# Optimization experiments

Hardware: AMD Instinct MI355X
Metric: run time of the kernel (lower is better)

The kernel has to match this reference:

```python
import jax, jax.numpy as jnp
import numpy as np

N_NODES, N_EDGES, D = 50000, 1250000, 64
N_LAYERS = 3


def setup_inputs() -> dict:
    key = jax.random.key(0)
    ks = jax.random.split(key, 6)
    sc = 1.0 / np.sqrt(D)  # ~xavier scale for 64->64 linears
    return {
        "in_feat": jax.random.normal(ks[0], (N_NODES, D), jnp.float32),
        "src": jax.random.randint(ks[1], (N_EDGES,), 0, N_NODES, dtype=jnp.int32),
        "dst": jax.random.randint(ks[2], (N_EDGES,), 0, N_NODES, dtype=jnp.int32),
        "W_pool": jax.random.normal(ks[3], (N_LAYERS, D, D), jnp.float32) * sc,
        "b_pool": jnp.zeros((N_LAYERS, D), jnp.float32),
        "W_self": jax.random.normal(ks[4], (N_LAYERS, D, D), jnp.float32) * sc,
        "W_neigh": jax.random.normal(ks[5], (N_LAYERS, D, D), jnp.float32) * sc,
        "bias": jnp.zeros((N_LAYERS, D), jnp.float32),
    }


def reference(in_feat, src, dst, W_pool, b_pool, W_self, W_neigh, bias):
    # Dropout is identity in eval mode and omitted for determinism.
    n = in_feat.shape[0]
    h = in_feat
    for l in range(N_LAYERS):
        # per-edge pool MLP: relu(W_pool h_src + b_pool)  -> [E, D]
        m = jax.nn.relu(h[src] @ W_pool[l] + b_pool[l])
        # max-pool aggregation over incoming edges of each dst node
        agg = jax.ops.segment_max(m, dst, num_segments=n)
        # nodes with no in-edges get -inf from segment_max -> DGL uses 0
        agg = jnp.where(jnp.isfinite(agg), agg, 0.0)
        h = h @ W_self[l] + agg @ W_neigh[l] + bias[l]
        if l < N_LAYERS - 1:
            h = jax.nn.relu(h)
    return h
```

## Files before the change

kernel.cpp:

```cpp
#include <hip/hip_runtime.h>


#define NN 50000
#define NE 1250000
#define DD 64

#define BSH 7
#define NB1 391
#define CHUNK 2048
#define NBLK1 611

#define GEMM_BLOCKS 782
#define CAST_BLOCKS 400
#define NMAT 9

using bf16x8 = __attribute__((ext_vector_type(8))) short;
using f32x4  = __attribute__((ext_vector_type(4))) float;

__device__ __forceinline__ f32x4 mfma16(bf16x8 a, bf16x8 b, f32x4 c) {
    return __builtin_amdgcn_mfma_f32_16x16x32_bf16(a, b, c, 0, 0, 0);
}

__device__ __forceinline__ unsigned int f32_to_bf16_bits(float f) {
    unsigned int u = __float_as_uint(f);
    return (u + 0x7FFFu + ((u >> 16) & 1u)) >> 16;
}
__device__ __forceinline__ unsigned int pack2bf16(float a, float b) {
    return f32_to_bf16_bits(a) | (f32_to_bf16_bits(b) << 16);
}
__device__ __forceinline__ unsigned int pkmax(unsigned int a, unsigned int b) {
    unsigned int r;
    asm("v_pk_max_u16 %0, %1, %2" : "=v"(r) : "v"(a), "v"(b));
    return r;
}

__device__ __forceinline__ void load_A(const unsigned short* __restrict__ h,
                                       int row0, int lane, bf16x8& a0, bf16x8& a1) {
    int r = row0 + (lane & 15);
    int kk = (lane >> 4) * 8;
    a0 = bf16x8{0, 0, 0, 0, 0, 0, 0, 0};
    a1 = a0;
    if (r < NN) {
        a0 = *(const bf16x8*)(h + (size_t)r * DD + kk);
        a1 = *(const bf16x8*)(h + (size_t)r * DD + kk + 32);
    }
}


__global__ __launch_bounds__(256) void fat1(const int* __restrict__ dst,
                                            int* __restrict__ H,
                                            const float* __restrict__ in_feat,
                                            unsigned short* __restrict__ h0,
                                            const float* __restrict__ Wp,
                                            const float* __restrict__ Ws,
                                            const float* __restrict__ Wn,
                                            unsigned short* __restrict__ wb) {
    __shared__ int hist[NB1];
    int tid = threadIdx.x;
    int bx = blockIdx.x;
    if (bx < NBLK1) {
        for (int i = tid; i < NB1; i += 256) hist[i] = 0;
        __syncthreads();
        int base = bx * CHUNK;
        int end = min(base + CHUNK, NE);
        for (int i = base + tid; i < end; i += 256) atomicAdd(&hist[dst[i] >> BSH], 1);
        __syncthreads();
        for (int k = tid; k < NB1; k += 256) H[k * NBLK1 + bx] = hist[k];
        return;
    }
    if (bx < NBLK1 + CAST_BLOCKS) {
        const float4* inv = (const float4*)in_feat;
        uint4* ov = (uint4*)h0;
        int t = (bx - NBLK1) * 256 + tid;
        for (int u = t; u < (NN * DD) / 8; u += CAST_BLOCKS * 256) {
            float4 f0 = inv[u * 2], f1 = inv[u * 2 + 1];
            uint4 o;
            o.x = pack2bf16(f0.x, f0.y);
            o.y = pack2bf16(f0.z, f0.w);
            o.z = pack2bf16(f1.x, f1.y);
            o.w = pack2bf16(f1.z, f1.w);
            ov[u] = o;
        }
        return;
    }
    int m = bx - NBLK1 - CAST_BLOCKS;
    const float* srcW = (m < 3) ? (Wp + (size_t)m * DD * DD)
                    : (m < 6) ? (Ws + (size_t)(m - 3) * DD * DD)
                              : (Wn + (size_t)(m - 6) * DD * DD);
    unsigned short* dstW = wb + (size_t)m * 512 * 8;
    for (int idx = tid; idx < 512; idx += 256) {
        int lane = idx & 63, cc = (idx >> 6) & 3, s = idx >> 8;
        int col = cc * 16 + (lane & 15);
        int kb = s * 32 + ((lane >> 4) << 3);
#pragma unroll
        for (int j = 0; j < 8; ++j)
            dstW[idx * 8 + j] = (unsigned short)f32_to_bf16_bits(srcW[(kb + j) * DD + col]);
    }
}


__global__ __launch_bounds__(256) void fat2(const int* __restrict__ H,
                                            int* __restrict__ rowsum,
                                            int* __restrict__ colbase,
                                            int* __restrict__ ticket,
                                            const unsigned short* __restrict__ h0,
                                            const unsigned short* __restrict__ wb,
                                            const float* __restrict__ bp,
                                            unsigned short* __restrict__ z) {
    __shared__ int s[256];
    __shared__ int isLast;
    int tid = threadIdx.x;
    int bx = blockIdx.x;
    if (bx < NB1) {
        int k = bx;
        int v = 0;
        for (int b = tid; b < NBLK1; b += 256) v += H[k * NBLK1 + b];
        s[tid] = v;
        __syncthreads();
        for (int o = 128; o > 0; o >>= 1) {
            if (tid < o) s[tid] += s[tid + o];
            __syncthreads();
        }
        if (tid == 0) {
            atomicExch(&rowsum[k], s[0]);
            __threadfence();
            isLast = (atomicAdd(ticket, 1) == NB1 - 1);
        }
        __syncthreads();
        if (!isLast) return;
        if (tid < 64) {
            int running = 0;
            for (int b0 = 0; b0 < NB1; b0 += 64) {
                int idx = b0 + tid;
                int val = (idx < NB1) ? atomicAdd(&rowsum[idx], 0) : 0;
                int incl = val;
#pragma unroll
                for (int o = 1; o < 64; o <<= 1) {
                    int up = __shfl_up(incl, o);
                    if (tid >= o) incl += up;
                }
                if (idx < NB1) colbase[idx] = running + (incl - val);
                running += __shfl(incl, 63);
            }
            if (tid == 0) colbase[NB1] = running;
        }
        return;
    }
    int lane = tid & 63;
    int row0 = (bx - NB1) * 64 + (tid >> 6) * 16;
    bf16x8 a0, a1;
    load_A(h0, row0, lane, a0, a1);
    const bf16x8* WB = (const bf16x8*)wb;
    f32x4 acc[4];
#pragma unroll
    for (int c = 0; c < 4; ++c) {
        float bv = bp[c * 16 + (lane & 15)];
        acc[c] = f32x4{bv, bv, bv, bv};
        acc[c] = mfma16(a0, WB[(0 * 4 + c) * 64 + lane], acc[c]);
        acc[c] = mfma16(a1, WB[(1 * 4 + c) * 64 + lane], acc[c]);
    }
    int rbase = row0 + (lane >> 4) * 4;
#pragma unroll
    for (int reg = 0; reg < 4; ++reg) {
        int row = rbase + reg;
        if (row < NN) {
#pragma unroll
            for (int c = 0; c < 4; ++c)
                z[(size_t)row * DD + c * 16 + (lane & 15)] =
                    (unsigned short)f32_to_bf16_bits(fmaxf(acc[c][reg], 0.f));
        }
    }
}


__global__ __launch_bounds__(256) void k3_offsets(int* __restrict__ H,
                                                  const int* __restrict__ colbase) {
    int wid = (blockIdx.x * blockDim.x + threadIdx.x) >> 6;
    int lane = threadIdx.x & 63;
    if (wid >= NB1) return;
    int running = colbase[wid];
    int* row = H + wid * NBLK1;
    for (int b0 = 0; b0 < NBLK1; b0 += 64) {
        int idx = b0 + lane;
        int v = (idx < NBLK1) ? row[idx] : 0;
        int incl = v;
#pragma unroll
        for (int o = 1; o < 64; o <<= 1) {
            int up = __shfl_up(incl, o);
            if (lane >= o) incl += up;
        }
        if (idx < NBLK1) row[idx] = running + (incl - v);
        running += __shfl(incl, 63);
    }
}

__global__ __launch_bounds__(512) void p1_scatter(const int* __restrict__ dst,
                                                  const int* __restrict__ src,
                                                  const int* __restrict__ H,
                                                  int* __restrict__ pairs, int e) {
    __shared__ int off[NB1];
    __shared__ int hcnt[NB1];
    __shared__ int cursor[NB1];
    __shared__ int lbase[NB1 + 1];
    __shared__ int sorted[CHUNK];
    __shared__ int sbuf[2][512];
    int tid = threadIdx.x, bx = blockIdx.x;
    for (int i = tid; i < NB1; i += 512) {
        off[i] = H[i * NBLK1 + bx];
        hcnt[i] = 0;
        cursor[i] = 0;
    }
    __syncthreads();
    int base = bx * CHUNK;
    int end = min(base + CHUNK, e);
    int L = end - base;
    for (int i = base + tid; i < end; i += 512) atomicAdd(&hcnt[dst[i] >> BSH], 1);
    __syncthreads();
    int myv = (tid < NB1) ? hcnt[tid] : 0;
    sbuf[0][tid] = myv;
    __syncthreads();
    int cur = 0;
    for (int o = 1; o < 512; o <<= 1) {
        sbuf[cur ^ 1][tid] = sbuf[cur][tid] + ((tid >= o) ? sbuf[cur][tid - o] : 0);
        cur ^= 1;
        __syncthreads();
    }
    if (tid < NB1) lbase[tid] = sbuf[cur][tid] - myv;
    if (tid == 0) lbase[NB1] = L;
    __syncthreads();
    for (int i = base + tid; i < end; i += 512) {
        int d = dst[i];
        int k = d >> BSH;
        int r = atomicAdd(&cursor[k], 1);
        sorted[lbase[k] + r] = ((d & 127) << 16) | src[i];
    }
    __syncthreads();
    for (int t = tid; t < L; t += 512) {
        int lo = 0, hi = NB1;
        while (hi - lo > 1) {
            int mid = (lo + hi) >> 1;
            if (t >= lbase[mid]) lo = mid; else hi = mid;
        }
        pairs[off[lo] + (t - lbase[lo])] = sorted[t];
    }
}

__global__ __launch_bounds__(512) void p2_bucket(const int* __restrict__ pairs,
                                                 const int* __restrict__ colbase,
                                                 int* __restrict__ rowptr,
                                                 unsigned short* __restrict__ edge_src) {
    __shared__ int cnt[128];
    __shared__ int base2[128];
    __shared__ int cur2[128];
    __shared__ int sbuf[2][128];
    __shared__ unsigned short stage[8192];
    int k = blockIdx.x;
    int tid = threadIdx.x;
    int beg = colbase[k], end = colbase[k + 1];
    int len = end - beg;
    if (tid < 128) { cnt[tid] = 0; cur2[tid] = 0; }
    __syncthreads();
    for (int i = beg + tid; i < end; i += 512) atomicAdd(&cnt[pairs[i] >> 16], 1);
    __syncthreads();
    if (tid < 128) sbuf[0][tid] = cnt[tid];
    __syncthreads();
    int cur = 0;
    for (int o = 1; o < 128; o <<= 1) {
        if (tid < 128) sbuf[cur ^ 1][tid] = sbuf[cur][tid] + ((tid >= o) ? sbuf[cur][tid - o] : 0);
        cur ^= 1;
        __syncthreads();
    }
    if (tid < 128) {
        int excl = sbuf[cur][tid] - cnt[tid];
        base2[tid] = excl;
        int node = (k << BSH) + tid;
        if (node < NN) rowptr[node] = beg + excl;
    }
    __syncthreads();
    if (len <= 8192) {
        for (int i = beg + tid; i < end; i += 512) {
            int p = pairs[i];
            int r = atomicAdd(&cur2[p >> 16], 1);
            stage[base2[p >> 16] + r] = (unsigned short)(p & 0xFFFF);
        }
        __syncthreads();
        for (int t = tid; t < len; t += 512) edge_src[beg + t] = stage[t];
    } else {
        for (int i = beg + tid; i < end; i += 512) {
            int p = pairs[i];
            int r = atomicAdd(&cur2[p >> 16], 1);
            edge_src[beg + base2[p >> 16] + r] = (unsigned short)(p & 0xFFFF);
        }
    }
    if (k == 0 && tid == 0) rowptr[NN] = NE;
}


__global__ __launch_bounds__(256) void gemm_fused_mfma(const unsigned short* __restrict__ h,
                                                       const unsigned short* __restrict__ agg,
                                                       const unsigned short* __restrict__ wbs,
                                                       const unsigned short* __restrict__ wbn,
                                                       const unsigned short* __restrict__ wbp,
                                                       const float* __restrict__ b,
                                                       const float* __restrict__ bp,
                                                       unsigned short* __restrict__ hn_out,
                                                       unsigned short* __restrict__ z) {
    __shared__ unsigned short hnl[4][16 * 72];
    int tid = threadIdx.x;
    int w = tid >> 6, lane = tid & 63;
    int row0 = blockIdx.x * 64 + w * 16;
    bf16x8 ah0, ah1, ag0, ag1;
    load_A(h, row0, lane, ah0, ah1);
    load_A(agg, row0, lane, ag0, ag1);
    const bf16x8* WS = (const bf16x8*)wbs;
    const bf16x8* WN = (const bf16x8*)wbn;
    const bf16x8* WP = (const bf16x8*)wbp;
    f32x4 acc[4];
#pragma unroll
    for (int c = 0; c < 4; ++c) {
        float bv = b[c * 16 + (lane & 15)];
        acc[c] = f32x4{bv, bv, bv, bv};
        acc[c] = mfma16(ah0, WS[(0 * 4 + c) * 64 + lane], acc[c]);
        acc[c] = mfma16(ah1, WS[(1 * 4 + c) * 64 + lane], acc[c]);
        acc[c] = mfma16(ag0, WN[(0 * 4 + c) * 64 + lane], acc[c]);
        acc[c] = mfma16(ag1, WN[(1 * 4 + c) * 64 + lane], acc[c]);
    }
    int rloc = (lane >> 4) * 4;
    int rbase = row0 + rloc;
#pragma unroll
    for (int reg = 0; reg < 4; ++reg) {
        int row = rbase + reg;
#pragma unroll
        for (int c = 0; c < 4; ++c) {
            unsigned short us =
                (unsigned short)f32_to_bf16_bits(fmaxf(acc[c][reg], 0.f));
            hnl[w][(rloc + reg) * 72 + c * 16 + (lane & 15)] = us;
            if (row < NN) hn_out[(size_t)row * DD + c * 16 + (lane & 15)] = us;
        }
    }
    int kk = (lane >> 4) * 8;
    bf16x8 p0 = *(const bf16x8*)&hnl[w][(lane & 15) * 72 + kk];
    bf16x8 p1 = *(const bf16x8*)&hnl[w][(lane & 15) * 72 + kk + 32];
    f32x4 acc2[4];
#pragma unroll
    for (int c = 0; c < 4; ++c) {
        float bv = bp[c * 16 + (lane & 15)];
        acc2[c] = f32x4{bv, bv, bv, bv};
        acc2[c] = mfma16(p0, WP[(0 * 4 + c) * 64 + lane], acc2[c]);
        acc2[c] = mfma16(p1, WP[(1 * 4 + c) * 64 + lane], acc2[c]);
    }
#pragma unroll
    for (int reg = 0; reg < 4; ++reg) {
        int row = rbase + reg;
        if (row < NN) {
#pragma unroll
            for (int c = 0; c < 4; ++c)
                z[(size_t)row * DD + c * 16 + (lane & 15)] =
                    (unsigned short)f32_to_bf16_bits(fmaxf(acc2[c][reg], 0.f));
        }
    }
}

__global__ __launch_bounds__(256) void gemm_final_mfma(const unsigned short* __restrict__ h,
                                                       const unsigned short* __restrict__ agg,
                                                       const unsigned short* __restrict__ wbs,
                                                       const unsigned short* __restrict__ wbn,
                                                       const float* __restrict__ b,
                                                       float* __restrict__ out) {
    int tid = threadIdx.x;
    int lane = tid & 63;
    int row0 = blockIdx.x * 64 + (tid >> 6) * 16;
    bf16x8 ah0, ah1, ag0, ag1;
    load_A(h, row0, lane, ah0, ah1);
    load_A(agg, row0, lane, ag0, ag1);
    const bf16x8* WS = (const bf16x8*)wbs;
    const bf16x8* WN = (const bf16x8*)wbn;
    f32x4 acc[4];
#pragma unroll
    for (int c = 0; c < 4; ++c) {
        float bv = b[c * 16 + (lane & 15)];
        acc[c] = f32x4{bv, bv, bv, bv};
        acc[c] = mfma16(ah0, WS[(0 * 4 + c) * 64 + lane], acc[c]);
        acc[c] = mfma16(ah1, WS[(1 * 4 + c) * 64 + lane], acc[c]);
        acc[c] = mfma16(ag0, WN[(0 * 4 + c) * 64 + lane], acc[c]);
        acc[c] = mfma16(ag1, WN[(1 * 4 + c) * 64 + lane], acc[c]);
    }
    int rbase = row0 + (lane >> 4) * 4;
#pragma unroll
    for (int reg = 0; reg < 4; ++reg) {
        int row = rbase + reg;
        if (row < NN) {
#pragma unroll
            for (int c = 0; c < 4; ++c)
                out[(size_t)row * DD + c * 16 + (lane & 15)] = acc[c][reg];
        }
    }
}


__global__ __launch_bounds__(256) void agg_max(const unsigned short* __restrict__ z,
                                               const int* __restrict__ rowptr,
                                               const unsigned short* __restrict__ edge_src,
                                               unsigned short* __restrict__ agg, int n) {
    int wslot = __builtin_amdgcn_readfirstlane((int)((blockIdx.x * blockDim.x + threadIdx.x) >> 6));
    int nslots = (gridDim.x * blockDim.x) >> 6;
    int lane = threadIdx.x & 63;
    int eg = lane >> 3;
    int fo = (lane & 7) * 8;
    for (int node = wslot; node < n; node += nslots) {
        int beg = rowptr[node];
        int end = rowptr[node + 1];
        unsigned int m0 = 0, m1 = 0, m2 = 0, m3 = 0;
        int e = beg;
#pragma unroll 2
        for (; e + 8 <= end; e += 8) {
            int s = edge_src[e + eg];
            uint4 a = *(const uint4*)(z + (size_t)s * DD + fo);
            m0 = pkmax(m0, a.x);
            m1 = pkmax(m1, a.y);
            m2 = pkmax(m2, a.z);
            m3 = pkmax(m3, a.w);
        }
        if (e + eg < end) {
            int s = edge_src[e + eg];
            uint4 a = *(const uint4*)(z + (size_t)s * DD + fo);
            m0 = pkmax(m0, a.x);
            m1 = pkmax(m1, a.y);
            m2 = pkmax(m2, a.z);
            m3 = pkmax(m3, a.w);
        }
#pragma unroll
        for (int o = 8; o < 64; o <<= 1) {
            m0 = pkmax(m0, (unsigned int)__shfl_xor((int)m0, o));
            m1 = pkmax(m1, (unsigned int)__shfl_xor((int)m1, o));
            m2 = pkmax(m2, (unsigned int)__shfl_xor((int)m2, o));
            m3 = pkmax(m3, (unsigned int)__shfl_xor((int)m3, o));
        }
        if (eg == 0) {
            uint4 o;
            o.x = m0; o.y = m1; o.z = m2; o.w = m3;
            *(uint4*)(agg + (size_t)node * DD + fo) = o;
        }
    }
}


extern "C" void kernel_launch(void* const* d_in, const int* in_sizes, int n_in,
                              void* d_out, int out_size, void* d_ws, size_t ws_size,
                              hipStream_t stream) {
    const float* in_feat = (const float*)d_in[0];
    const int* src = (const int*)d_in[1];
    const int* dst = (const int*)d_in[2];
    const float* W_pool = (const float*)d_in[3];
    const float* b_pool = (const float*)d_in[4];
    const float* W_self = (const float*)d_in[5];
    const float* W_neigh = (const float*)d_in[6];
    const float* bias = (const float*)d_in[7];
    float* out = (float*)d_out;

    char* ws = (char*)d_ws;
    size_t off = 0;
    auto alloc = [&](size_t bytes) -> void* {
        void* p = (void*)(ws + off);
        off += (bytes + 255) & ~(size_t)255;
        return p;
    };
    int* rowptr              = (int*)alloc((NN + 1) * sizeof(int));
    int* H                   = (int*)alloc((size_t)NB1 * NBLK1 * sizeof(int));
    int* rowsum              = (int*)alloc(NB1 * sizeof(int));
    int* colbase             = (int*)alloc((NB1 + 1) * sizeof(int));
    int* ticket              = (int*)alloc(sizeof(int));
    unsigned short* edge_src = (unsigned short*)alloc((size_t)NE * sizeof(unsigned short));
    unsigned short* z        = (unsigned short*)alloc((size_t)NN * DD * sizeof(unsigned short));
    unsigned short* agg      = (unsigned short*)alloc((size_t)NN * DD * sizeof(unsigned short));
    unsigned short* h0       = (unsigned short*)alloc((size_t)NN * DD * sizeof(unsigned short));
    unsigned short* h1       = (unsigned short*)alloc((size_t)NN * DD * sizeof(unsigned short));
    unsigned short* h2       = (unsigned short*)alloc((size_t)NN * DD * sizeof(unsigned short));
    unsigned short* wb       = (unsigned short*)alloc((size_t)NMAT * 512 * 8 * sizeof(unsigned short));
    int* pairs               = (int*)alloc((size_t)NE * sizeof(int));
    (void)ws_size; (void)in_sizes; (void)n_in; (void)out_size;

    hipMemsetAsync(ticket, 0, sizeof(int), stream);

    auto WBp = [&](int l) { return wb + (size_t)(0 + l) * 4096; };
    auto WBs = [&](int l) { return wb + (size_t)(3 + l) * 4096; };
    auto WBn = [&](int l) { return wb + (size_t)(6 + l) * 4096; };

    fat1<<<NBLK1 + CAST_BLOCKS + NMAT, 256, 0, stream>>>(
        dst, H, in_feat, h0, W_pool, W_self, W_neigh, wb);
    fat2<<<NB1 + GEMM_BLOCKS, 256, 0, stream>>>(
        H, rowsum, colbase, ticket, h0, wb, b_pool, z);
    k3_offsets<<<(NB1 * 64 + 255) / 256, 256, 0, stream>>>(H, colbase);
    p1_scatter<<<NBLK1, 512, 0, stream>>>(dst, src, H, pairs, NE);
    p2_bucket<<<NB1, 512, 0, stream>>>(pairs, colbase, rowptr, edge_src);

    agg_max<<<2048, 256, 0, stream>>>(z, rowptr, edge_src, agg, NN);
    gemm_fused_mfma<<<GEMM_BLOCKS, 256, 0, stream>>>(
        h0, agg, WBs(0), WBn(0), WBp(1), bias, b_pool + DD, h1, z);
    agg_max<<<2048, 256, 0, stream>>>(z, rowptr, edge_src, agg, NN);
    gemm_fused_mfma<<<GEMM_BLOCKS, 256, 0, stream>>>(
        h1, agg, WBs(1), WBn(1), WBp(2), bias + DD, b_pool + 2 * DD, h2, z);
    agg_max<<<2048, 256, 0, stream>>>(z, rowptr, edge_src, agg, NN);
    gemm_final_mfma<<<GEMM_BLOCKS, 256, 0, stream>>>(
        h2, agg, WBs(2), WBn(2), bias + 2 * DD, out);
}
```

Before: 166.4 us.

## Fuse layer-0 max aggregation into bucket sort kernel

The first agg_max launch is merged into the CSR bucketing kernel. Each block builds its 128-node segment, then reads edge sources from the LDS staging buffer, or from global memory when the bucket is too large, and computes the packed bf16 max over z for those nodes. This saves a kernel launch and a global re-read of rowptr and edge_src. The cost is that aggregation now runs on only 391 blocks of 512 threads instead of 2048 blocks, which may lower parallelism for the gather.

```diff
diff --git a/kernel.cpp b/kernel.cpp
--- a/kernel.cpp
+++ b/kernel.cpp
@@ -245,10 +245,12 @@
     }
 }
 
-__global__ __launch_bounds__(512) void p2_bucket(const int* __restrict__ pairs,
-                                                 const int* __restrict__ colbase,
-                                                 int* __restrict__ rowptr,
-                                                 unsigned short* __restrict__ edge_src) {
+__global__ __launch_bounds__(512) void p2_bucket_agg0(const int* __restrict__ pairs,
+                                                      const int* __restrict__ colbase,
+                                                      int* __restrict__ rowptr,
+                                                      unsigned short* __restrict__ edge_src,
+                                                      const unsigned short* __restrict__ z,
+                                                      unsigned short* __restrict__ agg) {
     __shared__ int cnt[128];
     __shared__ int base2[128];
     __shared__ int cur2[128];
@@ -277,7 +279,8 @@
         if (node < NN) rowptr[node] = beg + excl;
     }
     __syncthreads();
-    if (len <= 8192) {
+    int inLds = (len <= 8192);
+    if (inLds) {
         for (int i = beg + tid; i < end; i += 512) {
             int p = pairs[i];
             int r = atomicAdd(&cur2[p >> 16], 1);
@@ -291,8 +294,42 @@
             int r = atomicAdd(&cur2[p >> 16], 1);
             edge_src[beg + base2[p >> 16] + r] = (unsigned short)(p & 0xFFFF);
         }
+        __threadfence_block();
+        __syncthreads();
     }
     if (k == 0 && tid == 0) rowptr[NN] = NE;
+
+    int lane = tid & 63;
+    int w = tid >> 6;
+    int eg = lane >> 3;
+    int fo = (lane & 7) * 8;
+    for (int t = w; t < 128; t += 8) {
+        int node = (k << BSH) + t;
+        if (node >= NN) break;
+        int nb = base2[t];
+        int ecnt = cnt[t];
+        unsigned int m0 = 0, m1 = 0, m2 = 0, m3 = 0;
+        for (int e = eg; e < ecnt; e += 8) {
+            int s = inLds ? (int)stage[nb + e] : (int)edge_src[beg + nb + e];
+            uint4 a = *(const uint4*)(z + (size_t)s * DD + fo);
+            m0 = pkmax(m0, a.x);
+            m1 = pkmax(m1, a.y);
+            m2 = pkmax(m2, a.z);
+            m3 = pkmax(m3, a.w);
+        }
+#pragma unroll
+        for (int o = 8; o < 64; o <<= 1) {
+            m0 = pkmax(m0, (unsigned int)__shfl_xor((int)m0, o));
+            m1 = pkmax(m1, (unsigned int)__shfl_xor((int)m1, o));
+            m2 = pkmax(m2, (unsigned int)__shfl_xor((int)m2, o));
+            m3 = pkmax(m3, (unsigned int)__shfl_xor((int)m3, o));
+        }
+        if (eg == 0) {
+            uint4 o;
+            o.x = m0; o.y = m1; o.z = m2; o.w = m3;
+            *(uint4*)(agg + (size_t)node * DD + fo) = o;
+        }
+    }
 }
 
 
@@ -492,9 +529,8 @@
         H, rowsum, colbase, ticket, h0, wb, b_pool, z);
     k3_offsets<<<(NB1 * 64 + 255) / 256, 256, 0, stream>>>(H, colbase);
     p1_scatter<<<NBLK1, 512, 0, stream>>>(dst, src, H, pairs, NE);
-    p2_bucket<<<NB1, 512, 0, stream>>>(pairs, colbase, rowptr, edge_src);
-
-    agg_max<<<2048, 256, 0, stream>>>(z, rowptr, edge_src, agg, NN);
+    p2_bucket_agg0<<<NB1, 512, 0, stream>>>(pairs, colbase, rowptr, edge_src, z, agg);
+
     gemm_fused_mfma<<<GEMM_BLOCKS, 256, 0, stream>>>(
         h0, agg, WBs(0), WBn(0), WBp(1), bias, b_pool + DD, h1, z);
     agg_max<<<2048, 256, 0, stream>>>(z, rowptr, edge_src, agg, NN);
```

Result: slower. 174.3 us (+4.7%).
